# Optimization experiments

Hardware: AMD Instinct MI355X
Metric: run time of the kernel (lower is better)

## Reference

```python
import jax, jax.numpy as jnp
import numpy as np

B, N, D = 32, 512, 256
ITERATION_STEPS = 2


def setup_inputs() -> dict:
    key = jax.random.key(0)
    ks = jax.random.split(key, 20)
    node = jax.random.normal(ks[0], (B, N, D), dtype=jnp.float32)
    node_mask = jnp.ones((B, N), dtype=jnp.int32)
    graphs = [(jax.random.uniform(ks[1 + i], (B, N, N)) < 0.05).astype(jnp.int32)
              for i in range(6)]
    s = 0.02
    params = {
        'w_nw': jax.random.normal(ks[8], (D, 1)) * s,
        'b_nw': jnp.zeros((1,), jnp.float32),
        'w_self': jax.random.normal(ks[9], (D, D)) * s,
        'b_self': jnp.zeros((D,), jnp.float32),
        'w_arg1': jax.random.normal(ks[10], (D, D)) * s,
        'w_arg2': jax.random.normal(ks[11], (D, D)) * s,
        'w_arg3': jax.random.normal(ks[12], (D, D)) * s,
        'w_arg4': jax.random.normal(ks[13], (D, D)) * s,
        'w_punct': jax.random.normal(ks[14], (D, D)) * s,
        'w_punct_re': jax.random.normal(ks[15], (D, D)) * s,
    }
    return {'node': node, 'node_mask': node_mask,
            'arg_graph_1': graphs[0], 'arg_graph_2': graphs[1],
            'arg_graph_3': graphs[2], 'arg_graph_4': graphs[3],
            'punct_graph': graphs[4], 'punct_graph_re': graphs[5],
            **params}


def reference(node, node_mask, arg_graph_1, arg_graph_2, arg_graph_3, arg_graph_4,
              punct_graph, punct_graph_re,
              w_nw, b_nw, w_self, b_self,
              w_arg1, w_arg2, w_arg3, w_arg4, w_punct, w_punct_re):
    n = node.shape[1]
    diag = jnp.eye(n, dtype=node_mask.dtype)  # [N,N]
    # dd_graph: pairwise valid mask with zeroed diagonal, [B,N,N]
    dd = node_mask[:, None, :] * node_mask[:, :, None] * (1 - diag)
    G = jnp.stack([arg_graph_1, arg_graph_2, arg_graph_3, arg_graph_4,
                   punct_graph, punct_graph_re], 0) * dd[None]  # [6,B,N,N]
    Gf = G.astype(node.dtype)
    # neighbor count over all 6 edge types; replace 0 by 1 to avoid div-by-zero
    nn_num = Gf.sum(axis=(0, -1))  # [B,N]
    nn_num = jnp.where(nn_num >= 1, nn_num, jnp.ones_like(nn_num))
    W = jnp.stack([w_arg1, w_arg2, w_arg3, w_arg4, w_punct, w_punct_re], 0)  # [6,D,D]

    all_weight = []
    for _ in range(ITERATION_STEPS):
        # (1) node relatedness measure
        d_node_weight = jax.nn.sigmoid(node @ w_nw + b_nw)[..., 0]  # [B,N]
        all_weight.append(d_node_weight)
        self_node_info = node @ w_self + b_self  # [B,N,D]
        # (2) message propagation: per edge type k, project then aggregate
        proj = jnp.einsum('bnd,kde->kbne', node, W)            # [6,B,N,D]
        masked_w = d_node_weight[None, :, None, :] * Gf        # [6,B,N,N]
        agg = jnp.einsum('kbmn,kbne->bme', masked_w, proj)     # [B,N,D]
        # (3) update
        node = jax.nn.relu(self_node_info + agg / nn_num[..., None])
    return node, jnp.stack(all_weight, axis=1)  # [B,N,D], [B,steps,N]
```

## Files before the change

kernel.cpp:

```cpp
#include <hip/hip_runtime.h>

#define Bb 32
#define Nn 512
#define Dd 256
#define KC 1792
#define NR (Bb * Nn)

typedef __bf16 bf16x8 __attribute__((ext_vector_type(8)));
typedef float  f32x4  __attribute__((ext_vector_type(4)));
typedef int    i32x4  __attribute__((ext_vector_type(4)));
typedef unsigned short u16;

__device__ __forceinline__ u16 f2bf(float x){
  union { float f; unsigned u; } c; c.f = x;
  unsigned u = c.u;
  u += 0x7FFFu + ((u >> 16) & 1u);
  return (u16)(u >> 16);
}

__global__ __launch_bounds__(256) void k_prep(
    const float* __restrict__ wself,
    const float* __restrict__ w0, const float* __restrict__ w1,
    const float* __restrict__ w2, const float* __restrict__ w3,
    const float* __restrict__ w4, const float* __restrict__ w5,
    u16* __restrict__ wcatT){
  int e = blockIdx.x;
  const float* Ws[7] = {wself, w0, w1, w2, w3, w4, w5};
  for (int c = threadIdx.x; c < KC; c += 256){
    int g = c >> 8, j = c & 255;
    wcatT[(size_t)e*KC + c] = f2bf(Ws[g][j*Dd + e]);
  }
}

__global__ __launch_bounds__(256) void k_dw(
    const float* __restrict__ node, const int* __restrict__ mask,
    const float* __restrict__ wnw, const float* __restrict__ bnw,
    float* __restrict__ aw_out,
    u16* __restrict__ Nbf, u16* __restrict__ Xp){
  __shared__ float tile[32][268];
  __shared__ float dws[32];
  int b = blockIdx.x >> 4, n0 = (blockIdx.x & 15) << 5;
  int t = threadIdx.x;
  int row = t >> 3, seg = t & 7;
  const float* src = node + ((size_t)(b * Nn + n0 + row)) * Dd + seg * 32;
  u16* zn = Nbf + ((size_t)(b * Nn + n0 + row)) * Dd + seg * 32;
  #pragma unroll
  for (int c = 0; c < 8; ++c){
    float4 v = ((const float4*)src)[c];
    tile[row][seg * 32 + c * 4 + 0] = v.x;
    tile[row][seg * 32 + c * 4 + 1] = v.y;
    tile[row][seg * 32 + c * 4 + 2] = v.z;
    tile[row][seg * 32 + c * 4 + 3] = v.w;
    ushort4 h;
    h.x = f2bf(v.x); h.y = f2bf(v.y); h.z = f2bf(v.z); h.w = f2bf(v.w);
    ((ushort4*)zn)[c] = h;
  }
  __syncthreads();
  float s = 0.f;
  #pragma unroll
  for (int c = 0; c < 32; ++c) s += tile[row][seg * 32 + c] * wnw[seg * 32 + c];
  s += __shfl_xor(s, 1); s += __shfl_xor(s, 2); s += __shfl_xor(s, 4);
  if (seg == 0){
    float dw = 1.f / (1.f + expf(-(s + bnw[0])));
    aw_out[b * (2 * Nn) + n0 + row] = dw;
    dws[row] = mask[b * Nn + n0 + row] ? dw : 0.f;
  }
  __syncthreads();
  {
    float dwr = dws[row];
    u16* xp = Xp + ((size_t)(b * Nn + n0 + row)) * Dd + seg * 32;
    #pragma unroll
    for (int c = 0; c < 8; ++c){
      ushort4 h;
      h.x = f2bf(dwr * tile[row][seg * 32 + c * 4 + 0]);
      h.y = f2bf(dwr * tile[row][seg * 32 + c * 4 + 1]);
      h.z = f2bf(dwr * tile[row][seg * 32 + c * 4 + 2]);
      h.w = f2bf(dwr * tile[row][seg * 32 + c * 4 + 3]);
      ((ushort4*)xp)[c] = h;
    }
  }
}

__global__ __launch_bounds__(256) void k_ycat(
    const u16* __restrict__ Xp, const u16* __restrict__ wcatT,
    u16* __restrict__ Yt){
  int n0 = blockIdx.x * 128, c0 = blockIdx.y * 128, b = blockIdx.z;
  int kg = c0 >> 8, eg0 = c0 & 255;
  __shared__ u16 As[128 * 72];
  __shared__ u16 Bs[128 * 72];
  int t = threadIdx.x, lane = t & 63, wid = t >> 6;
  int wm = wid >> 1, wn = wid & 1;
  f32x4 acc[4][4];
  #pragma unroll
  for (int i = 0; i < 4; ++i)
    #pragma unroll
    for (int q = 0; q < 4; ++q) acc[i][q] = (f32x4){0.f, 0.f, 0.f, 0.f};

  for (int ks = 0; ks < 4; ++ks){
    int k0 = ks * 64;
    #pragma unroll
    for (int p = 0; p < 4; ++p){
      int row = p * 32 + (t >> 3);
      *(uint4*)&As[row * 72 + (t & 7) * 8] =
          *(const uint4*)(Xp + ((size_t)(b * Nn + n0 + row)) * Dd + k0 + (t & 7) * 8);
      *(uint4*)&Bs[row * 72 + (t & 7) * 8] =
          *(const uint4*)(wcatT + (size_t)(eg0 + row) * KC + 256 + kg * 256 + k0 + (t & 7) * 8);
    }
    __syncthreads();
    #pragma unroll
    for (int kk = 0; kk < 2; ++kk){
      bf16x8 av[4], bv[4];
      #pragma unroll
      for (int i = 0; i < 4; ++i)
        av[i] = *(const bf16x8*)&As[(wm * 64 + i * 16 + (lane & 15)) * 72 + kk * 32 + (lane >> 4) * 8];
      #pragma unroll
      for (int q = 0; q < 4; ++q)
        bv[q] = *(const bf16x8*)&Bs[(wn * 64 + q * 16 + (lane & 15)) * 72 + kk * 32 + (lane >> 4) * 8];
      #pragma unroll
      for (int i = 0; i < 4; ++i)
        #pragma unroll
        for (int q = 0; q < 4; ++q)
          acc[i][q] = __builtin_amdgcn_mfma_f32_16x16x32_bf16(av[i], bv[q], acc[i][q], 0, 0, 0);
    }
    __syncthreads();
  }
  #pragma unroll
  for (int i = 0; i < 4; ++i){
    int nbase = n0 + wm * 64 + i * 16 + (lane >> 4) * 4;
    #pragma unroll
    for (int q = 0; q < 4; ++q){
      int eg = eg0 + wn * 64 + q * 16 + (lane & 15);
      ushort4 h;
      h.x = f2bf(acc[i][q][0]); h.y = f2bf(acc[i][q][1]);
      h.z = f2bf(acc[i][q][2]); h.w = f2bf(acc[i][q][3]);
      *(ushort4*)(Yt + ((size_t)((b * 6 + kg) * 256 + eg)) * Nn + nbase) = h;
    }
  }
}

__global__ __launch_bounds__(256) void k_agg1(
    const int* __restrict__ g0, const int* __restrict__ g1,
    const int* __restrict__ g2, const int* __restrict__ g3,
    const int* __restrict__ g4, const int* __restrict__ g5,
    const int* __restrict__ mask, const u16* __restrict__ Yt,
    const u16* __restrict__ Nbf, const u16* __restrict__ wcatT,
    const float* __restrict__ bself,
    unsigned char* __restrict__ Gp8, float* __restrict__ rs,
    float* __restrict__ outp){
  __shared__ u16 As[32 * 72];
  __shared__ u16 BW[256 * 72];
  __shared__ int nns[32][9];
  __shared__ float rsl[32];
  __shared__ unsigned char lmask8[64];
  const int* gs[6] = {g0, g1, g2, g3, g4, g5};
  int id = blockIdx.x;
  int xcd = id & 7, q = id >> 3;
  int b = xcd * 4 + (q & 3), mt = q >> 2;
  int m0 = mt * 32;
  int t = threadIdx.x, lane = t & 63, wn = t >> 6;
  int arow = t >> 3, q8 = t & 7;
  int mloc = m0 + arow;

  if (t < 64){
    const int* mp = mask + (size_t)b * Nn + t * 8;
    unsigned mb = 0;
    #pragma unroll
    for (int j = 0; j < 8; ++j) mb |= (unsigned)(mp[j] & 1) << j;
    lmask8[t] = (unsigned char)mb;
  }
  __syncthreads();

  f32x4 acc[2][4];
  #pragma unroll
  for (int i = 0; i < 2; ++i)
    #pragma unroll
    for (int q2 = 0; q2 < 4; ++q2) acc[i][q2] = (f32x4){0.f, 0.f, 0.f, 0.f};

  int nnp = 0;
  for (int k = 0; k < 6; ++k){
    const int* Gk = gs[k] + ((size_t)(b * Nn + m0)) * Nn;
    const u16* Yk = Yt + ((size_t)((b * 6 + k) * 256)) * Nn;
    for (int ks = 0; ks < 8; ++ks){
      {
        const i32x4* gp = (const i32x4*)(Gk + (size_t)arow * Nn + ks * 64 + q8 * 8);
        i32x4 x0 = gp[0], x1 = gp[1];
        unsigned bits = (unsigned)((x0[0] & 1) | ((x0[1] & 1) << 1) |
                                   ((x0[2] & 1) << 2) | ((x0[3] & 1) << 3) |
                                   ((x1[0] & 1) << 4) | ((x1[1] & 1) << 5) |
                                   ((x1[2] & 1) << 6) | ((x1[3] & 1) << 7));
        unsigned dm = ((mloc >> 3) == (ks * 8 + q8)) ? (1u << (mloc & 7)) : 0u;
        bits &= ~dm;
        unsigned mb = lmask8[ks * 8 + q8];
        unsigned bm = bits & mb;
        nnp += __popc(bm);
        Gp8[(((size_t)k * NR + b * Nn + m0 + arow) * 16 + ks * 2 + (q8 >> 2)) * 4 + (q8 & 3)] =
            (unsigned char)bm;
        union { u16 h[8]; uint4 v; } pk;
        #pragma unroll
        for (int c = 0; c < 8; ++c)
          pk.h[c] = ((bits >> c) & 1u) ? 0x3F80 : 0;
        *(uint4*)&As[arow * 72 + q8 * 8] = pk.v;
      }
      #pragma unroll
      for (int p = 0; p < 8; ++p){
        int rowb = p * 32 + (t >> 3);
        *(uint4*)&BW[rowb * 72 + (t & 7) * 8] =
            *(const uint4*)(Yk + (size_t)rowb * Nn + ks * 64 + (t & 7) * 8);
      }
      __syncthreads();
      #pragma unroll
      for (int kk = 0; kk < 2; ++kk){
        bf16x8 av[2], bv[4];
        #pragma unroll
        for (int i = 0; i < 2; ++i)
          av[i] = *(const bf16x8*)&As[(i * 16 + (lane & 15)) * 72 + kk * 32 + (lane >> 4) * 8];
        #pragma unroll
        for (int q2 = 0; q2 < 4; ++q2)
          bv[q2] = *(const bf16x8*)&BW[(wn * 64 + q2 * 16 + (lane & 15)) * 72 + kk * 32 + (lane >> 4) * 8];
        #pragma unroll
        for (int i = 0; i < 2; ++i)
          #pragma unroll
          for (int q2 = 0; q2 < 4; ++q2)
            acc[i][q2] = __builtin_amdgcn_mfma_f32_16x16x32_bf16(av[i], bv[q2], acc[i][q2], 0, 0, 0);
      }
      __syncthreads();
    }
  }
  nns[arow][q8] = nnp;
  __syncthreads();
  if (t < 32){
    int s = 0;
    #pragma unroll
    for (int j = 0; j < 8; ++j) s += nns[t][j];
    int r = b * Nn + m0 + t;
    float v = mask[r] ? 1.0f / (float)(s < 1 ? 1 : s) : 0.0f;
    rsl[t] = v;
    rs[r] = v;
  }
  __syncthreads();
  #pragma unroll
  for (int i = 0; i < 2; ++i)
    #pragma unroll
    for (int rr = 0; rr < 4; ++rr){
      float s = rsl[i * 16 + (lane >> 4) * 4 + rr];
      #pragma unroll
      for (int q2 = 0; q2 < 4; ++q2) acc[i][q2][rr] *= s;
    }
  for (int ds = 0; ds < 4; ++ds){
    if (t < 256){
      *(uint4*)&As[(t >> 3) * 72 + (t & 7) * 8] =
          *(const uint4*)(Nbf + ((size_t)(b * Nn + m0 + (t >> 3))) * Dd + ds * 64 + (t & 7) * 8);
    }
    #pragma unroll
    for (int p = 0; p < 8; ++p){
      int rowb = p * 32 + (t >> 3);
      *(uint4*)&BW[rowb * 72 + (t & 7) * 8] =
          *(const uint4*)(wcatT + (size_t)rowb * KC + ds * 64 + (t & 7) * 8);
    }
    __syncthreads();
    #pragma unroll
    for (int kk = 0; kk < 2; ++kk){
      bf16x8 av[2], bv[4];
      #pragma unroll
      for (int i = 0; i < 2; ++i)
        av[i] = *(const bf16x8*)&As[(i * 16 + (lane & 15)) * 72 + kk * 32 + (lane >> 4) * 8];
      #pragma unroll
      for (int q2 = 0; q2 < 4; ++q2)
        bv[q2] = *(const bf16x8*)&BW[(wn * 64 + q2 * 16 + (lane & 15)) * 72 + kk * 32 + (lane >> 4) * 8];
      #pragma unroll
      for (int i = 0; i < 2; ++i)
        #pragma unroll
        for (int q2 = 0; q2 < 4; ++q2)
          acc[i][q2] = __builtin_amdgcn_mfma_f32_16x16x32_bf16(av[i], bv[q2], acc[i][q2], 0, 0, 0);
    }
    __syncthreads();
  }
  #pragma unroll
  for (int i = 0; i < 2; ++i){
    #pragma unroll
    for (int rr = 0; rr < 4; ++rr){
      size_t gr = (size_t)b * Nn + m0 + i * 16 + (lane >> 4) * 4 + rr;
      #pragma unroll
      for (int q2 = 0; q2 < 4; ++q2){
        int col = wn * 64 + q2 * 16 + (lane & 15);
        float v = acc[i][q2][rr] + bself[col];
        outp[gr * Dd + col] = v > 0.f ? v : 0.f;
      }
    }
  }
}

__global__ __launch_bounds__(256) void k_agg2(
    const unsigned* __restrict__ Gp, const u16* __restrict__ Yt,
    const u16* __restrict__ Nbf, const u16* __restrict__ wcatT,
    const float* __restrict__ rs, const float* __restrict__ bself,
    float* __restrict__ outp){
  __shared__ u16 As[64 * 72];
  __shared__ u16 BW[128 * 72];
  int id = blockIdx.x;
  int xcd = id & 7, q = id >> 3;
  int b = xcd * 4 + (q & 3), mt = (q >> 2) & 7, z = q >> 5;
  int m0 = mt * 64, e0 = z * 128;
  int t = threadIdx.x, lane = t & 63, wn = t >> 6;
  int arow = t >> 2, aq = t & 3;

  float rsv[16];
  #pragma unroll
  for (int i = 0; i < 4; ++i)
    #pragma unroll
    for (int r = 0; r < 4; ++r)
      rsv[i * 4 + r] = rs[b * Nn + m0 + i * 16 + (lane >> 4) * 4 + r];

  f32x4 accA[4][2];
  #pragma unroll
  for (int i = 0; i < 4; ++i)
    #pragma unroll
    for (int q2 = 0; q2 < 2; ++q2)
      accA[i][q2] = (f32x4){0.f, 0.f, 0.f, 0.f};

  for (int k = 0; k < 6; ++k){
    const unsigned* Gr = Gp + ((size_t)k * NR + b * Nn + m0) * 16;
    unsigned wpre[8];
    #pragma unroll
    for (int ks2 = 0; ks2 < 8; ++ks2)
      wpre[ks2] = Gr[arow * 16 + ks2 * 2 + (aq >> 1)];
    const u16* Yk = Yt + ((size_t)((b * 6 + k) * 256)) * Nn;

    for (int ks2 = 0; ks2 < 8; ++ks2){
      {
        unsigned bits = (wpre[ks2] >> ((aq & 1) * 16)) & 0xFFFFu;
        union { u16 h[16]; uint4 v[2]; } pk;
        #pragma unroll
        for (int c = 0; c < 16; ++c)
          pk.h[c] = ((bits >> c) & 1u) ? 0x3F80 : 0;
        *(uint4*)&As[arow * 72 + aq * 16]     = pk.v[0];
        *(uint4*)&As[arow * 72 + aq * 16 + 8] = pk.v[1];
      }
      #pragma unroll
      for (int p = 0; p < 4; ++p){
        int rowb = p * 32 + (t >> 3);
        *(uint4*)&BW[rowb * 72 + (t & 7) * 8] =
            *(const uint4*)(Yk + (size_t)(e0 + rowb) * Nn + ks2 * 64 + (t & 7) * 8);
      }
      __syncthreads();
      #pragma unroll
      for (int kk = 0; kk < 2; ++kk){
        bf16x8 av[4], bv[2];
        #pragma unroll
        for (int i = 0; i < 4; ++i)
          av[i] = *(const bf16x8*)&As[(i * 16 + (lane & 15)) * 72 + kk * 32 + (lane >> 4) * 8];
        #pragma unroll
        for (int q2 = 0; q2 < 2; ++q2)
          bv[q2] = *(const bf16x8*)&BW[(wn * 32 + q2 * 16 + (lane & 15)) * 72 + kk * 32 + (lane >> 4) * 8];
        #pragma unroll
        for (int i = 0; i < 4; ++i)
          #pragma unroll
          for (int q2 = 0; q2 < 2; ++q2)
            accA[i][q2] = __builtin_amdgcn_mfma_f32_16x16x32_bf16(av[i], bv[q2], accA[i][q2], 0, 0, 0);
      }
      __syncthreads();
    }
  }
  #pragma unroll
  for (int i = 0; i < 4; ++i)
    #pragma unroll
    for (int rr = 0; rr < 4; ++rr){
      float s = rsv[i * 4 + rr];
      #pragma unroll
      for (int q2 = 0; q2 < 2; ++q2) accA[i][q2][rr] *= s;
    }
  for (int ds = 0; ds < 4; ++ds){
    #pragma unroll
    for (int p = 0; p < 2; ++p){
      int row = p * 32 + (t >> 3);
      *(uint4*)&As[row * 72 + (t & 7) * 8] =
          *(const uint4*)(Nbf + ((size_t)(b * Nn + m0 + row)) * Dd + ds * 64 + (t & 7) * 8);
    }
    #pragma unroll
    for (int p = 0; p < 4; ++p){
      int rowb = p * 32 + (t >> 3);
      *(uint4*)&BW[rowb * 72 + (t & 7) * 8] =
          *(const uint4*)(wcatT + (size_t)(e0 + rowb) * KC + ds * 64 + (t & 7) * 8);
    }
    __syncthreads();
    #pragma unroll
    for (int kk = 0; kk < 2; ++kk){
      bf16x8 av[4], bv[2];
      #pragma unroll
      for (int i = 0; i < 4; ++i)
        av[i] = *(const bf16x8*)&As[(i * 16 + (lane & 15)) * 72 + kk * 32 + (lane >> 4) * 8];
      #pragma unroll
      for (int q2 = 0; q2 < 2; ++q2)
        bv[q2] = *(const bf16x8*)&BW[(wn * 32 + q2 * 16 + (lane & 15)) * 72 + kk * 32 + (lane >> 4) * 8];
      #pragma unroll
      for (int i = 0; i < 4; ++i)
        #pragma unroll
        for (int q2 = 0; q2 < 2; ++q2)
          accA[i][q2] = __builtin_amdgcn_mfma_f32_16x16x32_bf16(av[i], bv[q2], accA[i][q2], 0, 0, 0);
    }
    __syncthreads();
  }
  #pragma unroll
  for (int i = 0; i < 4; ++i){
    #pragma unroll
    for (int rr = 0; rr < 4; ++rr){
      size_t gr = (size_t)b * Nn + m0 + i * 16 + (lane >> 4) * 4 + rr;
      #pragma unroll
      for (int q2 = 0; q2 < 2; ++q2){
        int col = e0 + wn * 32 + q2 * 16 + (lane & 15);
        float v = accA[i][q2][rr] + bself[col];
        outp[gr * Dd + col] = v > 0.f ? v : 0.f;
      }
    }
  }
}

extern "C" void kernel_launch(void* const* d_in, const int* in_sizes, int n_in,
                              void* d_out, int out_size, void* d_ws, size_t ws_size,
                              hipStream_t stream){
  (void)in_sizes; (void)n_in; (void)out_size; (void)ws_size;
  const float* node  = (const float*)d_in[0];
  const int*   mask  = (const int*)d_in[1];
  const int*   g[6];
  for (int i = 0; i < 6; ++i) g[i] = (const int*)d_in[2 + i];
  const float* wnw   = (const float*)d_in[8];
  const float* bnw   = (const float*)d_in[9];
  const float* wself = (const float*)d_in[10];
  const float* bself = (const float*)d_in[11];
  const float* W[6];
  for (int i = 0; i < 6; ++i) W[i] = (const float*)d_in[12 + i];

  float* out_node = (float*)d_out;
  float* out_aw   = out_node + (size_t)Bb * Nn * Dd;

  char* ws = (char*)d_ws;
  u16*      wcatT = (u16*)(ws);
  float*    rs    = (float*)(ws + 917504);
  unsigned* Gp    = (unsigned*)(ws + 1048576);
  u16*      Xp    = (u16*)(ws + 7340032);
  u16*      Nbf   = (u16*)(ws + 15728640);
  u16*      Yt    = (u16*)(ws + 24117248);

  k_prep<<<256, 256, 0, stream>>>(wself, W[0], W[1], W[2], W[3], W[4], W[5], wcatT);

  k_dw<<<512, 256, 0, stream>>>(node, mask, wnw, bnw, out_aw, Nbf, Xp);
  k_ycat<<<dim3(4, 12, 32), 256, 0, stream>>>(Xp, wcatT, Yt);
  k_agg1<<<512, 256, 0, stream>>>(g[0], g[1], g[2], g[3], g[4], g[5], mask,
                                  Yt, Nbf, wcatT, bself,
                                  (unsigned char*)Gp, rs, out_node);

  k_dw<<<512, 256, 0, stream>>>(out_node, mask, wnw, bnw, out_aw + Nn, Nbf, Xp);
  k_ycat<<<dim3(4, 12, 32), 256, 0, stream>>>(Xp, wcatT, Yt);
  k_agg2<<<512, 256, 0, stream>>>(Gp, Yt, Nbf, wcatT, rs, bself, out_node);
}
```

Baseline: 242.5 us.

## Double-buffer LDS tiles in k_agg2 and stage graph bitmasks in shared memory

Flattens the 6x8 edge-type/k-step loops of the aggregation kernel into one 48-step loop. Each step fills the next A/B tile into the second buffer while MFMAs consume the current one, which removes one of the two barriers per step. All six edge-type bitmask slices are preloaded into LDS once at kernel start instead of being reloaded per edge type. In exchange the kernel uses more LDS, which may reduce occupancy, and the overlap depends on the compiler scheduling the global loads early.

After: 246.8 us. About the same (+1.8%).

```diff
diff --git a/kernel.cpp b/kernel.cpp
--- a/kernel.cpp
+++ b/kernel.cpp
@@ -295,8 +295,9 @@
     const u16* __restrict__ Nbf, const u16* __restrict__ wcatT,
     const float* __restrict__ rs, const float* __restrict__ bself,
     float* __restrict__ outp){
-  __shared__ u16 As[64 * 72];
-  __shared__ u16 BW[128 * 72];
+  __shared__ u16 As[2][64 * 72];
+  __shared__ u16 BW[2][128 * 72];
+  __shared__ unsigned Gq[6][64][16];
   int id = blockIdx.x;
   int xcd = id & 7, q = id >> 3;
   int b = xcd * 4 + (q & 3), mt = (q >> 2) & 7, z = q >> 5;
@@ -311,6 +312,13 @@
     for (int r = 0; r < 4; ++r)
       rsv[i * 4 + r] = rs[b * Nn + m0 + i * 16 + (lane >> 4) * 4 + r];
 
+  #pragma unroll
+  for (int k = 0; k < 6; ++k){
+    const uint4* src = (const uint4*)(Gp + ((size_t)k * NR + b * Nn + m0) * 16) + t;
+    *(uint4*)&Gq[k][t >> 2][(t & 3) * 4] = *src;
+  }
+  __syncthreads();
+
   f32x4 accA[4][2];
   #pragma unroll
   for (int i = 0; i < 4; ++i)
@@ -318,49 +326,47 @@
     for (int q2 = 0; q2 < 2; ++q2)
       accA[i][q2] = (f32x4){0.f, 0.f, 0.f, 0.f};
 
-  for (int k = 0; k < 6; ++k){
-    const unsigned* Gr = Gp + ((size_t)k * NR + b * Nn + m0) * 16;
-    unsigned wpre[8];
-    #pragma unroll
-    for (int ks2 = 0; ks2 < 8; ++ks2)
-      wpre[ks2] = Gr[arow * 16 + ks2 * 2 + (aq >> 1)];
-    const u16* Yk = Yt + ((size_t)((b * 6 + k) * 256)) * Nn;
-
-    for (int ks2 = 0; ks2 < 8; ++ks2){
-      {
-        unsigned bits = (wpre[ks2] >> ((aq & 1) * 16)) & 0xFFFFu;
-        union { u16 h[16]; uint4 v[2]; } pk;
-        #pragma unroll
-        for (int c = 0; c < 16; ++c)
-          pk.h[c] = ((bits >> c) & 1u) ? 0x3F80 : 0;
-        *(uint4*)&As[arow * 72 + aq * 16]     = pk.v[0];
-        *(uint4*)&As[arow * 72 + aq * 16 + 8] = pk.v[1];
-      }
-      #pragma unroll
-      for (int p = 0; p < 4; ++p){
-        int rowb = p * 32 + (t >> 3);
-        *(uint4*)&BW[rowb * 72 + (t & 7) * 8] =
-            *(const uint4*)(Yk + (size_t)(e0 + rowb) * Nn + ks2 * 64 + (t & 7) * 8);
-      }
-      __syncthreads();
-      #pragma unroll
-      for (int kk = 0; kk < 2; ++kk){
-        bf16x8 av[4], bv[2];
-        #pragma unroll
-        for (int i = 0; i < 4; ++i)
-          av[i] = *(const bf16x8*)&As[(i * 16 + (lane & 15)) * 72 + kk * 32 + (lane >> 4) * 8];
+#define STG(S, B) { int kk_ = (S) >> 3, k8_ = (S) & 7; \
+    unsigned w_ = Gq[kk_][arow][k8_ * 2 + (aq >> 1)]; \
+    unsigned bits = (w_ >> ((aq & 1) * 16)) & 0xFFFFu; \
+    union { u16 h[16]; uint4 v[2]; } pk_; \
+    _Pragma("unroll") \
+    for (int c = 0; c < 16; ++c) pk_.h[c] = ((bits >> c) & 1u) ? 0x3F80 : 0; \
+    *(uint4*)&As[B][arow * 72 + aq * 16]     = pk_.v[0]; \
+    *(uint4*)&As[B][arow * 72 + aq * 16 + 8] = pk_.v[1]; \
+    const u16* Yk_ = Yt + ((size_t)((b * 6 + kk_) * 256 + e0)) * Nn + k8_ * 64; \
+    _Pragma("unroll") \
+    for (int p = 0; p < 4; ++p){ \
+      int rowb = p * 32 + (t >> 3); \
+      *(uint4*)&BW[B][rowb * 72 + (t & 7) * 8] = \
+          *(const uint4*)(Yk_ + (size_t)rowb * Nn + (t & 7) * 8); \
+    } }
+
+  STG(0, 0);
+  __syncthreads();
+  int cur = 0;
+  for (int s = 0; s < 48; ++s){
+    if (s < 47) STG(s + 1, cur ^ 1);
+    #pragma unroll
+    for (int kk = 0; kk < 2; ++kk){
+      bf16x8 av[4], bv[2];
+      #pragma unroll
+      for (int i = 0; i < 4; ++i)
+        av[i] = *(const bf16x8*)&As[cur][(i * 16 + (lane & 15)) * 72 + kk * 32 + (lane >> 4) * 8];
+      #pragma unroll
+      for (int q2 = 0; q2 < 2; ++q2)
+        bv[q2] = *(const bf16x8*)&BW[cur][(wn * 32 + q2 * 16 + (lane & 15)) * 72 + kk * 32 + (lane >> 4) * 8];
+      #pragma unroll
+      for (int i = 0; i < 4; ++i)
         #pragma unroll
         for (int q2 = 0; q2 < 2; ++q2)
-          bv[q2] = *(const bf16x8*)&BW[(wn * 32 + q2 * 16 + (lane & 15)) * 72 + kk * 32 + (lane >> 4) * 8];
-        #pragma unroll
-        for (int i = 0; i < 4; ++i)
-          #pragma unroll
-          for (int q2 = 0; q2 < 2; ++q2)
-            accA[i][q2] = __builtin_amdgcn_mfma_f32_16x16x32_bf16(av[i], bv[q2], accA[i][q2], 0, 0, 0);
-      }
-      __syncthreads();
-    }
-  }
+          accA[i][q2] = __builtin_amdgcn_mfma_f32_16x16x32_bf16(av[i], bv[q2], accA[i][q2], 0, 0, 0);
+    }
+    __syncthreads();
+    cur ^= 1;
+  }
+#undef STG
+
   #pragma unroll
   for (int i = 0; i < 4; ++i)
     #pragma unroll
@@ -373,13 +379,13 @@
     #pragma unroll
     for (int p = 0; p < 2; ++p){
       int row = p * 32 + (t >> 3);
-      *(uint4*)&As[row * 72 + (t & 7) * 8] =
+      *(uint4*)&As[0][row * 72 + (t & 7) * 8] =
           *(const uint4*)(Nbf + ((size_t)(b * Nn + m0 + row)) * Dd + ds * 64 + (t & 7) * 8);
     }
     #pragma unroll
     for (int p = 0; p < 4; ++p){
       int rowb = p * 32 + (t >> 3);
-      *(uint4*)&BW[rowb * 72 + (t & 7) * 8] =
+      *(uint4*)&BW[0][rowb * 72 + (t & 7) * 8] =
           *(const uint4*)(wcatT + (size_t)(e0 + rowb) * KC + ds * 64 + (t & 7) * 8);
     }
     __syncthreads();
@@ -388,10 +394,10 @@
       bf16x8 av[4], bv[2];
       #pragma unroll
       for (int i = 0; i < 4; ++i)
-        av[i] = *(const bf16x8*)&As[(i * 16 + (lane & 15)) * 72 + kk * 32 + (lane >> 4) * 8];
+        av[i] = *(const bf16x8*)&As[0][(i * 16 + (lane & 15)) * 72 + kk * 32 + (lane >> 4) * 8];
       #pragma unroll
       for (int q2 = 0; q2 < 2; ++q2)
-        bv[q2] = *(const bf16x8*)&BW[(wn * 32 + q2 * 16 + (lane & 15)) * 72 + kk * 32 + (lane >> 4) * 8];
+        bv[q2] = *(const bf16x8*)&BW[0][(wn * 32 + q2 * 16 + (lane & 15)) * 72 + kk * 32 + (lane >> 4) * 8];
       #pragma unroll
       for (int i = 0; i < 4; ++i)
         #pragma unroll
```
